# Optimization experiments

Measured on AMD Instinct MI355X. Metric: run time of the kernel, lower is better.

Reference implementation:

```python
import jax, jax.numpy as jnp
import numpy as np

ALPHA = 0.2  # LeakyReLU negative slope
NEG = -9e15  # mask value from original code


def setup_inputs() -> dict:
    key = jax.random.key(0)
    k1, k2, k3, k4 = jax.random.split(key, 4)
    N, F_in, F_out = 8192, 256, 128
    h = jax.random.normal(k1, (N, F_in), dtype=jnp.float32)
    adj = jax.random.randint(k2, (N, N), 0, 2, dtype=jnp.int32)
    # xavier-ish scaled params
    W = jax.random.normal(k3, (F_out, F_in), dtype=jnp.float32) * (1.0 / np.sqrt(F_in))
    a = jax.random.normal(k4, (1, 2 * F_out), dtype=jnp.float32) * (1.0 / np.sqrt(2 * F_out))
    return {"h": h, "adj": adj, "W": W, "a": a}


def reference(h, adj, W, a):
    # Wh: [N, F_out]
    Wh = h @ W.T
    F_out = Wh.shape[1]
    # Algebraic decomposition of the pairwise-concat score:
    # e[i,j] = leakyrelu(a . [Wh_i ; Wh_j]) = leakyrelu(f1_i + f2_j)
    a1 = a[0, :F_out]   # [F_out]
    a2 = a[0, F_out:]   # [F_out]
    f1 = Wh @ a1        # [N]
    f2 = Wh @ a2        # [N]
    e = jax.nn.leaky_relu(f1[:, None] + f2[None, :], negative_slope=ALPHA)  # [N, N]
    scores = jnp.where(adj > 0, e, NEG)
    attention = jax.nn.softmax(scores, axis=1)  # dropout omitted (eval mode)
    return attention @ Wh  # [N, F_out]
```

## Files before the change

kernel.cpp:

```cpp
#include <hip/hip_runtime.h>
#include <hip/hip_bf16.h>


typedef __bf16 bf16;
typedef __attribute__((ext_vector_type(8))) __bf16 bf16x8;
typedef __attribute__((ext_vector_type(4))) float f32x4;
typedef __attribute__((ext_vector_type(4))) int i32x4;

#define NN 8192
#define F_IN 256
#define F_OUT 128
#define LOG2E 1.44269504088896f
#define ALPHA 0.2f
#define KSLICES 8

__device__ __forceinline__ void split8(const float* __restrict__ p,
                                       bf16x8& hi, bf16x8& lo) {
    const float4 u = *(const float4*)p;
    const float4 v = *(const float4*)(p + 4);
    float f[8] = {u.x, u.y, u.z, u.w, v.x, v.y, v.z, v.w};
#pragma unroll
    for (int j = 0; j < 8; ++j) {
        const bf16 h = (bf16)f[j];
        hi[j] = h;
        lo[j] = (bf16)(f[j] - (float)h);
    }
}

__global__ __launch_bounds__(256) void gat_whpack(
        const int* __restrict__ adj,
        const float* __restrict__ h,
        const float* __restrict__ W,
        const float* __restrict__ a,
        unsigned char* __restrict__ maskP,
        bf16* __restrict__ WhT,
        float* __restrict__ f1L,
        float* __restrict__ f2L) {
    const int tid = threadIdx.x;

    if (blockIdx.x >= 128) {
        const int row = (blockIdx.x - 128) * 4 + (tid >> 6);
        const int l = tid & 63;
        const int* rowp = adj + (size_t)row * NN;

#pragma unroll 4
        for (int iter = 0; iter < 16; ++iter) {
            const int base = iter * 512;
            const i32x4 v1 =
                __builtin_nontemporal_load((const i32x4*)(rowp + base + l * 4));
            const i32x4 v2 =
                __builtin_nontemporal_load((const i32x4*)(rowp + base + 256 + l * 4));
            unsigned int n1 = (v1[0] > 0 ? 1u : 0u) | (v1[1] > 0 ? 2u : 0u) |
                              (v1[2] > 0 ? 4u : 0u) | (v1[3] > 0 ? 8u : 0u);
            unsigned int n2 = (v2[0] > 0 ? 1u : 0u) | (v2[1] > 0 ? 2u : 0u) |
                              (v2[2] > 0 ? 4u : 0u) | (v2[3] > 0 ? 8u : 0u);
            const unsigned int p1 = __shfl_xor(n1, 1);
            const unsigned int p2 = __shfl_xor(n2, 1);
            if ((l & 1) == 0) {
                const int b1 = iter * 64 + (l >> 1);
                const int b2 = b1 + 32;
                maskP[((size_t)(b1 >> 7) << 20) + (size_t)row * 128 + (b1 & 127)] =
                    (unsigned char)(n1 | (p1 << 4));
                maskP[((size_t)(b2 >> 7) << 20) + (size_t)row * 128 + (b2 & 127)] =
                    (unsigned char)(n2 | (p2 << 4));
            }
        }
        return;
    }

    const int wb = blockIdx.x;
    const int wv = tid >> 6;
    const int l15 = tid & 15;
    const int g = (tid & 63) >> 4;
    const int rowbase = wb * 64 + wv * 16;

    f32x4 acc[8];
    const f32x4 zz = {0.f, 0.f, 0.f, 0.f};
#pragma unroll
    for (int nf = 0; nf < 8; ++nf) acc[nf] = zz;

#pragma unroll
    for (int ks = 0; ks < 8; ++ks) {
        const int k = ks * 32 + g * 8;
        bf16x8 ah, al;
        split8(h + (size_t)(rowbase + l15) * F_IN + k, ah, al);
#pragma unroll
        for (int nf = 0; nf < 8; ++nf) {
            bf16x8 bh, bl;
            split8(W + (size_t)(nf * 16 + l15) * F_IN + k, bh, bl);
            acc[nf] = __builtin_amdgcn_mfma_f32_16x16x32_bf16(ah, bh, acc[nf], 0, 0, 0);
            acc[nf] = __builtin_amdgcn_mfma_f32_16x16x32_bf16(ah, bl, acc[nf], 0, 0, 0);
            acc[nf] = __builtin_amdgcn_mfma_f32_16x16x32_bf16(al, bh, acc[nf], 0, 0, 0);
        }
    }

#pragma unroll
    for (int nf = 0; nf < 8; ++nf)
#pragma unroll
        for (int r = 0; r < 4; ++r)
            WhT[(size_t)(nf * 16 + l15) * NN + rowbase + g * 4 + r] = (bf16)acc[nf][r];

    float a1c[8], a2c[8];
#pragma unroll
    for (int nf = 0; nf < 8; ++nf) {
        a1c[nf] = a[nf * 16 + l15];
        a2c[nf] = a[F_OUT + nf * 16 + l15];
    }
#pragma unroll
    for (int r = 0; r < 4; ++r) {
        float s1 = 0.f, s2 = 0.f;
#pragma unroll
        for (int nf = 0; nf < 8; ++nf) {
            s1 += acc[nf][r] * a1c[nf];
            s2 += acc[nf][r] * a2c[nf];
        }
        s1 += __shfl_xor(s1, 1, 16);
        s1 += __shfl_xor(s1, 2, 16);
        s1 += __shfl_xor(s1, 4, 16);
        s1 += __shfl_xor(s1, 8, 16);
        s2 += __shfl_xor(s2, 1, 16);
        s2 += __shfl_xor(s2, 2, 16);
        s2 += __shfl_xor(s2, 4, 16);
        s2 += __shfl_xor(s2, 8, 16);
        if (l15 == 0) {
            f1L[rowbase + g * 4 + r] = s1 * LOG2E;
            f2L[rowbase + g * 4 + r] = s2 * LOG2E;
        }
    }
}

__global__ __launch_bounds__(512, 4) void gat_flash6(
        const unsigned char* __restrict__ maskP,
        const bf16* __restrict__ WhT,
        const float* __restrict__ f1L,
        const float* __restrict__ f2L,
        float* __restrict__ O_part,
        float* __restrict__ rs_part) {
    __shared__ __align__(16) char lds[39424];

    const int tid = threadIdx.x;
    const int wv = tid >> 6;
    const int l = tid & 63;
    const int l15 = l & 15;
    const int g = l >> 4;
    const int rb = blockIdx.x >> 3;
    const int ks = blockIdx.x & 7;
    const int row0 = rb * 128;
    const int lrow = wv * 16 + l15;

    const float f1a = f1L[row0 + lrow];

    const int mr = tid >> 2;
    const int mseg = tid & 3;
    const unsigned char* msrc =
        maskP + ((size_t)ks << 20) + (size_t)(row0 + mr) * 128 + mseg * 4;

    f32x4 acc[8];
    const f32x4 zz = {0.f, 0.f, 0.f, 0.f};
#pragma unroll
    for (int nf = 0; nf < 8; ++nf) acc[nf] = zz;
    float rs0 = 0.f;

    {
        const float2 v = *(const float2*)(f2L + ks * 1024 + tid * 2);
        *(float2*)(lds + 35328 + tid * 8) = v;
    }

    for (int it = 0; it < 8; ++it) {
        __syncthreads();
        const unsigned int mw = *(const unsigned int*)(msrc + it * 16);
        *(unsigned int*)(lds + 32768 + mr * 20 + mseg * 4) = mw;
#pragma unroll
        for (int j = 0; j < 4; ++j) {
            const int u = j * 512 + tid;
            const int cc = u >> 4;
            const int ku = u & 15;
            const bf16x8 v =
                *(const bf16x8*)(WhT + (size_t)cc * NN + ks * 1024 + it * 128 + ku * 8);
            *(bf16x8*)(lds + ((cc * 256 + ku * 16) ^ ((cc & 7) << 4))) = v;
        }
        __syncthreads();

#pragma unroll
        for (int s = 0; s < 4; ++s) {
            const unsigned int mb =
                *(const unsigned char*)(lds + 32768 + lrow * 20 + s * 4 + g);
            const int t = it * 4 + s;
            const float4 fa = *(const float4*)(lds + 35328 + t * 128 + g * 32);
            const float4 fb = *(const float4*)(lds + 35328 + t * 128 + g * 32 + 16);
            const float ff[8] = {fa.x, fa.y, fa.z, fa.w, fb.x, fb.y, fb.z, fb.w};

            bf16x8 pa;
#pragma unroll
            for (int j = 0; j < 8; ++j) {
                const float x = f1a + ff[j];
                const float e = __builtin_amdgcn_exp2f(fmaxf(x, ALPHA * x));
                pa[j] = (bf16)((mb & (1u << j)) ? e : 0.f);
            }
#pragma unroll
            for (int j = 0; j < 8; ++j) rs0 += (float)pa[j];

            __builtin_amdgcn_s_setprio(1);
#pragma unroll
            for (int nf = 0; nf < 8; ++nf) {
                const int c = nf * 16 + l15;
                const bf16x8 bh = *(const bf16x8*)(
                    lds + ((c * 256 + s * 64 + g * 16) ^ ((c & 7) << 4)));
                acc[nf] = __builtin_amdgcn_mfma_f32_16x16x32_bf16(pa, bh, acc[nf], 0, 0, 0);
            }
            __builtin_amdgcn_s_setprio(0);
        }
    }

    rs0 += __shfl_xor(rs0, 16);
    rs0 += __shfl_xor(rs0, 32);
    if (l < 16) rs_part[(size_t)ks * NN + row0 + lrow] = rs0;

    float* accL = (float*)lds;
#pragma unroll
    for (int half = 0; half < 2; ++half) {
        __syncthreads();
        if ((wv >> 2) == half) {
            const int rbase = (wv & 3) * 16;
#pragma unroll
            for (int nf = 0; nf < 8; ++nf)
#pragma unroll
                for (int r = 0; r < 4; ++r)
                    accL[(rbase + g * 4 + r) * 132 + nf * 16 + l15] = acc[nf][r];
        }
        __syncthreads();
        const int rr = tid >> 3;
        const int seg = tid & 7;
        float* dst = O_part + ((size_t)ks << 20) +
                     (size_t)(row0 + half * 64 + rr) * F_OUT + seg * 16;
        const float* src = accL + rr * 132 + seg * 16;
        *(float4*)(dst + 0) = *(const float4*)(src + 0);
        *(float4*)(dst + 4) = *(const float4*)(src + 4);
        *(float4*)(dst + 8) = *(const float4*)(src + 8);
        *(float4*)(dst + 12) = *(const float4*)(src + 12);
    }
}

__global__ __launch_bounds__(256) void gat_reduce(const float* __restrict__ O_part,
                                                  const float* __restrict__ rs_part,
                                                  float* __restrict__ out) {
    const int idx = blockIdx.x * 256 + threadIdx.x;
    const int r = idx >> 5;
    const int c = (idx & 31) * 4;
    float rsum = 0.f;
#pragma unroll
    for (int s = 0; s < KSLICES; ++s) rsum += rs_part[(size_t)s * NN + r];
    float4 o = {0.f, 0.f, 0.f, 0.f};
#pragma unroll
    for (int s = 0; s < KSLICES; ++s) {
        const float4 v =
            *(const float4*)(O_part + ((size_t)s << 20) + (size_t)r * F_OUT + c);
        o.x += v.x;
        o.y += v.y;
        o.z += v.z;
        o.w += v.w;
    }
    const float inv = 1.0f / rsum;
    o.x *= inv;
    o.y *= inv;
    o.z *= inv;
    o.w *= inv;
    *(float4*)(out + (size_t)r * F_OUT + c) = o;
}

extern "C" void kernel_launch(void* const* d_in, const int* in_sizes, int n_in,
                              void* d_out, int out_size, void* d_ws, size_t ws_size,
                              hipStream_t stream) {
    const float* h = (const float*)d_in[0];
    const int* adj = (const int*)d_in[1];
    const float* W = (const float*)d_in[2];
    const float* a = (const float*)d_in[3];
    float* out = (float*)d_out;

    char* ws = (char*)d_ws;
    const size_t MB = 1024 * 1024;
    bf16* WhT = (bf16*)ws;
    float* f1L = (float*)(ws + 2 * MB);
    float* f2L = f1L + NN;
    unsigned char* maskP = (unsigned char*)(ws + 3 * MB);
    float* rs_part = (float*)(ws + 11 * MB);
    float* O_part = (float*)(ws + 12 * MB);

    gat_whpack<<<2176, 256, 0, stream>>>(adj, h, W, a, maskP, WhT, f1L, f2L);
    gat_flash6<<<512, 512, 0, stream>>>(maskP, WhT, f1L, f2L, O_part, rs_part);
    gat_reduce<<<NN * F_OUT / 4 / 256, 256, 0, stream>>>(O_part, rs_part, out);
}
```

Before: 105.7 us.

## Switch flash attention kernel to 32x32x16 MFMA tiles with 4 waves

The main attention kernel now uses 32x32x16 bf16 MFMA instructions with 256-thread blocks, so each wave owns 32 rows instead of 16. The mask, f2 and Wh tile loading, the accumulator layout and the output write-back are remapped to match. Larger MFMA tiles reuse each LDS-loaded B fragment across more rows and halve the exp/mask work per instruction issued. The cost is fewer waves per block and more accumulator registers per lane, which may lower occupancy.

```diff
diff --git a/kernel.cpp b/kernel.cpp
--- a/kernel.cpp
+++ b/kernel.cpp
@@ -5,6 +5,7 @@
 typedef __bf16 bf16;
 typedef __attribute__((ext_vector_type(8))) __bf16 bf16x8;
 typedef __attribute__((ext_vector_type(4))) float f32x4;
+typedef __attribute__((ext_vector_type(16))) float f32x16;
 typedef __attribute__((ext_vector_type(4))) int i32x4;
 
 #define NN 8192
@@ -129,7 +130,7 @@
     }
 }
 
-__global__ __launch_bounds__(512, 4) void gat_flash6(
+__global__ __launch_bounds__(256, 4) void gat_flash632(
         const unsigned char* __restrict__ maskP,
         const bf16* __restrict__ WhT,
         const float* __restrict__ f1L,
@@ -141,38 +142,39 @@
     const int tid = threadIdx.x;
     const int wv = tid >> 6;
     const int l = tid & 63;
-    const int l15 = l & 15;
-    const int g = l >> 4;
+    const int l31 = l & 31;
+    const int jg = l >> 5;
     const int rb = blockIdx.x >> 3;
     const int ks = blockIdx.x & 7;
     const int row0 = rb * 128;
-    const int lrow = wv * 16 + l15;
+    const int lrow = wv * 32 + l31;
 
     const float f1a = f1L[row0 + lrow];
 
-    const int mr = tid >> 2;
-    const int mseg = tid & 3;
+    const int mr = tid >> 1;
+    const int mh = (tid & 1) * 8;
     const unsigned char* msrc =
-        maskP + ((size_t)ks << 20) + (size_t)(row0 + mr) * 128 + mseg * 4;
-
-    f32x4 acc[8];
-    const f32x4 zz = {0.f, 0.f, 0.f, 0.f};
-#pragma unroll
-    for (int nf = 0; nf < 8; ++nf) acc[nf] = zz;
+        maskP + ((size_t)ks << 20) + (size_t)(row0 + mr) * 128 + mh;
+
+    f32x16 acc[4];
+#pragma unroll
+    for (int ct = 0; ct < 4; ++ct)
+#pragma unroll
+        for (int e = 0; e < 16; ++e) acc[ct][e] = 0.f;
     float rs0 = 0.f;
 
     {
-        const float2 v = *(const float2*)(f2L + ks * 1024 + tid * 2);
-        *(float2*)(lds + 35328 + tid * 8) = v;
+        const float4 v = *(const float4*)(f2L + ks * 1024 + tid * 4);
+        *(float4*)(lds + 35328 + tid * 16) = v;
     }
 
     for (int it = 0; it < 8; ++it) {
         __syncthreads();
-        const unsigned int mw = *(const unsigned int*)(msrc + it * 16);
-        *(unsigned int*)(lds + 32768 + mr * 20 + mseg * 4) = mw;
-#pragma unroll
-        for (int j = 0; j < 4; ++j) {
-            const int u = j * 512 + tid;
+        const unsigned long long mw = *(const unsigned long long*)(msrc + it * 16);
+        *(unsigned long long*)(lds + 32768 + mr * 20 + mh) = mw;
+#pragma unroll
+        for (int j = 0; j < 8; ++j) {
+            const int u = j * 256 + tid;
             const int cc = u >> 4;
             const int ku = u & 15;
             const bf16x8 v =
@@ -182,12 +184,12 @@
         __syncthreads();
 
 #pragma unroll
-        for (int s = 0; s < 4; ++s) {
+        for (int s = 0; s < 8; ++s) {
             const unsigned int mb =
-                *(const unsigned char*)(lds + 32768 + lrow * 20 + s * 4 + g);
-            const int t = it * 4 + s;
-            const float4 fa = *(const float4*)(lds + 35328 + t * 128 + g * 32);
-            const float4 fb = *(const float4*)(lds + 35328 + t * 128 + g * 32 + 16);
+                *(const unsigned char*)(lds + 32768 + lrow * 20 + s * 2 + jg);
+            const int koff = (it * 128 + s * 16 + jg * 8) * 4;
+            const float4 fa = *(const float4*)(lds + 35328 + koff);
+            const float4 fb = *(const float4*)(lds + 35328 + koff + 16);
             const float ff[8] = {fa.x, fa.y, fa.z, fa.w, fb.x, fb.y, fb.z, fb.w};
 
             bf16x8 pa;
@@ -202,42 +204,42 @@
 
             __builtin_amdgcn_s_setprio(1);
 #pragma unroll
-            for (int nf = 0; nf < 8; ++nf) {
-                const int c = nf * 16 + l15;
+            for (int ct = 0; ct < 4; ++ct) {
+                const int c = ct * 32 + l31;
                 const bf16x8 bh = *(const bf16x8*)(
-                    lds + ((c * 256 + s * 64 + g * 16) ^ ((c & 7) << 4)));
-                acc[nf] = __builtin_amdgcn_mfma_f32_16x16x32_bf16(pa, bh, acc[nf], 0, 0, 0);
+                    lds + ((c * 256 + s * 32 + jg * 16) ^ ((c & 7) << 4)));
+                acc[ct] = __builtin_amdgcn_mfma_f32_32x32x16_bf16(pa, bh, acc[ct], 0, 0, 0);
             }
             __builtin_amdgcn_s_setprio(0);
         }
     }
 
-    rs0 += __shfl_xor(rs0, 16);
     rs0 += __shfl_xor(rs0, 32);
-    if (l < 16) rs_part[(size_t)ks * NN + row0 + lrow] = rs0;
+    if (l < 32) rs_part[(size_t)ks * NN + row0 + wv * 32 + l31] = rs0;
 
     float* accL = (float*)lds;
 #pragma unroll
-    for (int half = 0; half < 2; ++half) {
-        __syncthreads();
-        if ((wv >> 2) == half) {
-            const int rbase = (wv & 3) * 16;
-#pragma unroll
-            for (int nf = 0; nf < 8; ++nf)
-#pragma unroll
-                for (int r = 0; r < 4; ++r)
-                    accL[(rbase + g * 4 + r) * 132 + nf * 16 + l15] = acc[nf][r];
-        }
-        __syncthreads();
-        const int rr = tid >> 3;
-        const int seg = tid & 7;
+    for (int hh = 0; hh < 2; ++hh) {
+        __syncthreads();
+        if ((wv >> 1) == hh) {
+            const int rbase = (wv & 1) * 32;
+#pragma unroll
+            for (int ct = 0; ct < 4; ++ct)
+#pragma unroll
+                for (int r = 0; r < 16; ++r) {
+                    const int rloc = (r & 3) + 8 * (r >> 2) + 4 * jg;
+                    accL[(rbase + rloc) * 132 + ct * 32 + l31] = acc[ct][r];
+                }
+        }
+        __syncthreads();
+        const int rr = tid >> 2;
+        const int seg = tid & 3;
         float* dst = O_part + ((size_t)ks << 20) +
-                     (size_t)(row0 + half * 64 + rr) * F_OUT + seg * 16;
-        const float* src = accL + rr * 132 + seg * 16;
-        *(float4*)(dst + 0) = *(const float4*)(src + 0);
-        *(float4*)(dst + 4) = *(const float4*)(src + 4);
-        *(float4*)(dst + 8) = *(const float4*)(src + 8);
-        *(float4*)(dst + 12) = *(const float4*)(src + 12);
+                     (size_t)(row0 + hh * 64 + rr) * F_OUT + seg * 32;
+        const float* src = accL + rr * 132 + seg * 32;
+#pragma unroll
+        for (int j = 0; j < 8; ++j)
+            *(float4*)(dst + j * 4) = *(const float4*)(src + j * 4);
     }
 }
 
@@ -287,6 +289,6 @@
     float* O_part = (float*)(ws + 12 * MB);
 
     gat_whpack<<<2176, 256, 0, stream>>>(adj, h, W, a, maskP, WhT, f1L, f2L);
-    gat_flash6<<<512, 512, 0, stream>>>(maskP, WhT, f1L, f2L, O_part, rs_part);
+    gat_flash632<<<512, 256, 0, stream>>>(maskP, WhT, f1L, f2L, O_part, rs_part);
     gat_reduce<<<NN * F_OUT / 4 / 256, 256, 0, stream>>>(O_part, rs_part, out);
 }
```

After: 120.5 us. 1.14x slower.
